# Performance work log

Hardware: AMD Instinct MI355X
Metric: run time of the kernel (lower is better)

The kernel has to match this reference:

```python
import jax, jax.numpy as jnp
import numpy as np

B, Tt, Ta, Tv = 2048, 128, 256, 256
D, E, R, H, L, NC = 64, 4, 8, 4, 4, 7
SCALING = 16.0 / 8.0  # alpha / r


def _ln(x, g, b, eps=1e-5):
    m = x.mean(-1, keepdims=True)
    v = ((x - m) ** 2).mean(-1, keepdims=True)
    return (x - m) / jnp.sqrt(v + eps) * g + b


def setup_inputs() -> dict:
    key = jax.random.key(0)
    ks = iter(jax.random.split(key, 64))
    def rn(shape, s=0.05):
        return jax.random.normal(next(ks), shape, jnp.float32) * s
    d = {}
    d['text'] = jax.random.normal(next(ks), (B, Tt, 300), jnp.float32)
    d['audio'] = jax.random.normal(next(ks), (B, Ta, 74), jnp.float32)
    d['video'] = jax.random.normal(next(ks), (B, Tv, 35), jnp.float32)
    # modality projections (Linear + LayerNorm)
    d['text_w'] = rn((300, D)); d['text_b'] = jnp.zeros(D); d['text_ln_g'] = jnp.ones(D); d['text_ln_b'] = jnp.zeros(D)
    d['audio_w'] = rn((74, D)); d['audio_b'] = jnp.zeros(D); d['audio_ln_g'] = jnp.ones(D); d['audio_ln_b'] = jnp.zeros(D)
    d['video_w'] = rn((35, D)); d['video_b'] = jnp.zeros(D); d['video_ln_g'] = jnp.ones(D); d['video_ln_b'] = jnp.zeros(D)
    d['latent'] = rn((1, L, D), 0.02)
    # cross-attention in/out projections
    d['wq'] = rn((D, D)); d['bq'] = jnp.zeros(D)
    d['wk'] = rn((D, D)); d['bk'] = jnp.zeros(D)
    d['wv'] = rn((D, D)); d['bv'] = jnp.zeros(D)
    d['wo'] = rn((D, D)); d['bo'] = jnp.zeros(D)
    d['n1_g'] = jnp.ones(D); d['n1_b'] = jnp.zeros(D)
    d['ffn_w1'] = rn((D, 4 * D)); d['ffn_b1'] = jnp.zeros(4 * D)
    d['ffn_w2'] = rn((4 * D, D)); d['ffn_b2'] = jnp.zeros(D)
    d['n2_g'] = jnp.ones(D); d['n2_b'] = jnp.zeros(D)
    # router
    d['r_w1'] = rn((D, D)); d['r_b1'] = jnp.zeros(D)
    d['r_ln_g'] = jnp.ones(D); d['r_ln_b'] = jnp.zeros(D)
    d['r_w2'] = rn((D, E)); d['r_b2'] = jnp.zeros(E)
    d['p1_w'] = rn((D, D // 2)); d['p1_b'] = jnp.zeros(D // 2)
    d['p2_w'] = rn((D, D // 2)); d['p2_b'] = jnp.zeros(D // 2)
    # LoRA experts, stacked: down [E,D,R], up [E,R,D]
    d['lora_down'] = rn((E, D, R), 0.1)
    d['lora_up'] = rn((E, R, D), 0.1)
    # classifier
    d['c_ln_g'] = jnp.ones(D); d['c_ln_b'] = jnp.zeros(D)
    d['c_w1'] = rn((D, D), 0.02); d['c_b1'] = jnp.zeros(D)
    d['c_w2'] = rn((D, NC), 0.02); d['c_b2'] = jnp.zeros(NC)
    return d


def reference(text, audio, video,
              text_w, text_b, text_ln_g, text_ln_b,
              audio_w, audio_b, audio_ln_g, audio_ln_b,
              video_w, video_b, video_ln_g, video_ln_b,
              latent, wq, bq, wk, bk, wv, bv, wo, bo,
              n1_g, n1_b, ffn_w1, ffn_b1, ffn_w2, ffn_b2, n2_g, n2_b,
              r_w1, r_b1, r_ln_g, r_ln_b, r_w2, r_b2,
              p1_w, p1_b, p2_w, p2_b,
              lora_down, lora_up,
              c_ln_g, c_ln_b, c_w1, c_b1, c_w2, c_b2):
    b = text.shape[0]
    def proj(x, w, bb, g, gb):  # Linear + LN + ReLU (dropout = eval identity)
        return jax.nn.relu(_ln(x @ w + bb, g, gb))
    # mean-pool each modality over time, project to d_model -> [b,3,D]
    zt = proj(text.mean(1), text_w, text_b, text_ln_g, text_ln_b)
    za = proj(audio.mean(1), audio_w, audio_b, audio_ln_g, audio_ln_b)
    zv = proj(video.mean(1), video_w, video_b, video_ln_g, video_ln_b)
    inputs = jnp.stack([zt, za, zv], axis=1)  # [b,3,D]
    lat = jnp.broadcast_to(latent, (b, L, D))
    # cross-attention: latent queries attend over 3 modality tokens
    hd = D // H
    q = (lat @ wq + bq).reshape(b, L, H, hd)
    k = (inputs @ wk + bk).reshape(b, -1, H, hd)
    v = (inputs @ wv + bv).reshape(b, -1, H, hd)
    scores = jnp.einsum('blhd,bshd->bhls', q, k) / jnp.sqrt(jnp.float32(hd))
    attn = jax.nn.softmax(scores, axis=-1)
    attn_out = jnp.einsum('bhls,bshd->blhd', attn, v).reshape(b, L, D) @ wo + bo
    lat = _ln(lat + attn_out, n1_g, n1_b)
    ffn = jax.nn.gelu(lat @ ffn_w1 + ffn_b1, approximate=False) @ ffn_w2 + ffn_b2
    lat = _ln(lat + ffn, n2_g, n2_b)
    f = lat.mean(1)  # [b,D] perceiver features
    # router
    r_logits = jax.nn.relu(_ln(f @ r_w1 + r_b1, r_ln_g, r_ln_b)) @ r_w2 + r_b2
    weights = jax.nn.softmax(r_logits, axis=-1)  # [b,E]
    view1 = f @ p1_w + p1_b
    view2 = f @ p2_w + p2_b
    # all LoRA experts as one batched grouped GEMM
    down = jnp.einsum('bd,edr->ber', f, lora_down)
    up = jnp.einsum('ber,erd->bed', down, lora_up) * SCALING
    expert_out = f[:, None, :] + up  # [b,E,D]
    fused = jnp.einsum('bed,be->bd', expert_out, weights)
    # classifier
    h = jax.nn.relu(_ln(fused, c_ln_g, c_ln_b) @ c_w1 + c_b1)
    logits = h @ c_w2 + c_b2
    return (logits, weights, fused, f, view1, view2)
```

## Files before the change

### kernel.cpp

```cpp
#include <hip/hip_runtime.h>
#include <math.h>
#include <string.h>

#define B_   2048
#define TT   128
#define TA   256
#define TV   256
#define CT   300
#define CA   74
#define CV   35
#define D    64
#define E_   4
#define R_   8
#define H_   4
#define L_   4
#define NC   7
#define POOLW 416

struct Params {
  const float *text, *audio, *video;
  const float *text_w, *text_b, *text_ln_g, *text_ln_b;
  const float *audio_w, *audio_b, *audio_ln_g, *audio_ln_b;
  const float *video_w, *video_b, *video_ln_g, *video_ln_b;
  const float *latent;
  const float *wq, *bq, *wk, *bk, *wv, *bv, *wo, *bo;
  const float *n1_g, *n1_b, *ffn_w1, *ffn_b1, *ffn_w2, *ffn_b2, *n2_g, *n2_b;
  const float *r_w1, *r_b1, *r_ln_g, *r_ln_b, *r_w2, *r_b2;
  const float *p1_w, *p1_b, *p2_w, *p2_b;
  const float *lora_down, *lora_up;
  const float *c_ln_g, *c_ln_b, *c_w1, *c_b1, *c_w2, *c_b2;
  float *out;
};

__device__ __forceinline__ float wsum(float v) {
#pragma unroll
  for (int m = 32; m >= 1; m >>= 1) v += __shfl_xor(v, m, 64);
  return v;
}
__device__ __forceinline__ float hsum16(float v) {
#pragma unroll
  for (int m = 8; m >= 1; m >>= 1) v += __shfl_xor(v, m, 64);
  return v;
}
#define WB() __builtin_amdgcn_wave_barrier()

__global__ __launch_bounds__(256) void fused_kernel(Params p) {
  const int tid = threadIdx.x;
  const int lane = tid & 63;
  const int w = tid >> 6;
  const int b0 = blockIdx.x * 4;
  const int b = b0 + w;

  __shared__ __align__(16) float4 sbufT[3][4][75];
  __shared__ __align__(8)  float2 sbufA[6][4][37];
  __shared__ float sbufV[7][4][35];
  __shared__ __align__(16) float s_pool[4][POOLW];
  __shared__ float s_q[L_ * D];
  __shared__ float s_z[4][3 * D];
  __shared__ float s_k[4][3 * D];
  __shared__ float s_ao[4][L_ * D];
  __shared__ float s_lat1[4][L_ * D];
  __shared__ float s_h1w[4][256];
  __shared__ float s_f[4][D];
  __shared__ float s_down[4][E_ * R_];
  __shared__ float s_cl[4][D];

  {
    const int c4 = tid % 75, g = tid / 75;
    if (g < 3) {
      float4 acc[4];
#pragma unroll
      for (int s = 0; s < 4; ++s) acc[s] = make_float4(0.f, 0.f, 0.f, 0.f);
      for (int t = g; t < TT; t += 3) {
#pragma unroll
        for (int s = 0; s < 4; ++s) {
          float4 v = *reinterpret_cast<const float4*>(
              p.text + (size_t)(b0 + s) * (TT * CT) + t * CT + 4 * c4);
          acc[s].x += v.x; acc[s].y += v.y; acc[s].z += v.z; acc[s].w += v.w;
        }
      }
#pragma unroll
      for (int s = 0; s < 4; ++s) sbufT[g][s][c4] = acc[s];
    }
  }
  {
    const int c2 = tid % 37, g = tid / 37;
    if (g < 6) {
      float2 acc[4];
#pragma unroll
      for (int s = 0; s < 4; ++s) acc[s] = make_float2(0.f, 0.f);
      for (int t = g; t < TA; t += 6) {
#pragma unroll
        for (int s = 0; s < 4; ++s) {
          float2 v = *reinterpret_cast<const float2*>(
              p.audio + (size_t)(b0 + s) * (TA * CA) + t * CA + 2 * c2);
          acc[s].x += v.x; acc[s].y += v.y;
        }
      }
#pragma unroll
      for (int s = 0; s < 4; ++s) sbufA[g][s][c2] = acc[s];
    }
  }
  {
    const int c = tid % 35, g = tid / 35;
    if (g < 7) {
      float acc[4] = {0.f, 0.f, 0.f, 0.f};
      for (int t = g; t < TV; t += 7) {
#pragma unroll
        for (int s = 0; s < 4; ++s)
          acc[s] += p.video[(size_t)(b0 + s) * (TV * CV) + t * CV + c];
      }
#pragma unroll
      for (int s = 0; s < 4; ++s) sbufV[g][s][c] = acc[s];
    }
  }
  {
    const int l = tid >> 6, j = tid & 63;
    float acc = p.bq[j];
    for (int i = 0; i < D; ++i) acc += p.latent[l * D + i] * p.wq[i * D + j];
    s_q[tid] = acc;
  }
  __syncthreads();

  if (tid < 75) {
#pragma unroll
    for (int s = 0; s < 4; ++s) {
      float4 a = sbufT[0][s][tid], bb = sbufT[1][s][tid], c = sbufT[2][s][tid];
      float4 r;
      r.x = (a.x + bb.x + c.x) * (1.f / TT);
      r.y = (a.y + bb.y + c.y) * (1.f / TT);
      r.z = (a.z + bb.z + c.z) * (1.f / TT);
      r.w = (a.w + bb.w + c.w) * (1.f / TT);
      *reinterpret_cast<float4*>(&s_pool[s][4 * tid]) = r;
    }
  } else if (tid < 112) {
    const int c2 = tid - 75;
#pragma unroll
    for (int s = 0; s < 4; ++s) {
      float2 r = make_float2(0.f, 0.f);
#pragma unroll
      for (int g = 0; g < 6; ++g) { float2 v = sbufA[g][s][c2]; r.x += v.x; r.y += v.y; }
      r.x *= (1.f / TA); r.y *= (1.f / TA);
      *reinterpret_cast<float2*>(&s_pool[s][CT + 2 * c2]) = r;
    }
  } else if (tid < 147) {
    const int c = tid - 112;
#pragma unroll
    for (int s = 0; s < 4; ++s) {
      float r = 0.f;
#pragma unroll
      for (int g = 0; g < 7; ++g) r += sbufV[g][s][c];
      s_pool[s][CT + CA + c] = r * (1.f / TV);
    }
  }
  __syncthreads();

  {
    float acc = p.text_b[lane];
    for (int i = 0; i < CT; ++i) acc += s_pool[w][i] * p.text_w[i * D + lane];
    float mu = wsum(acc) * (1.f / D);
    float d = acc - mu;
    float var = wsum(d * d) * (1.f / D);
    s_z[w][0 * D + lane] =
        fmaxf(d * rsqrtf(var + 1e-5f) * p.text_ln_g[lane] + p.text_ln_b[lane], 0.f);

    acc = p.audio_b[lane];
    for (int i = 0; i < CA; ++i) acc += s_pool[w][CT + i] * p.audio_w[i * D + lane];
    mu = wsum(acc) * (1.f / D); d = acc - mu; var = wsum(d * d) * (1.f / D);
    s_z[w][1 * D + lane] =
        fmaxf(d * rsqrtf(var + 1e-5f) * p.audio_ln_g[lane] + p.audio_ln_b[lane], 0.f);

    acc = p.video_b[lane];
    for (int i = 0; i < CV; ++i) acc += s_pool[w][CT + CA + i] * p.video_w[i * D + lane];
    mu = wsum(acc) * (1.f / D); d = acc - mu; var = wsum(d * d) * (1.f / D);
    s_z[w][2 * D + lane] =
        fmaxf(d * rsqrtf(var + 1e-5f) * p.video_ln_g[lane] + p.video_ln_b[lane], 0.f);
  }
  WB();

  float vreg[3];
#pragma unroll
  for (int s = 0; s < 3; ++s) {
    float ak = p.bk[lane], av = p.bv[lane];
    for (int i = 0; i < D; ++i) {
      float z = s_z[w][s * D + i];
      ak += z * p.wk[i * D + lane];
      av += z * p.wv[i * D + lane];
    }
    s_k[w][s * D + lane] = ak;
    vreg[s] = av;
  }
  WB();

  float aw[L_][3];
#pragma unroll
  for (int l = 0; l < L_; ++l) {
    float sc0 = hsum16(s_q[l * D + lane] * s_k[w][0 * D + lane]) * 0.25f;
    float sc1 = hsum16(s_q[l * D + lane] * s_k[w][1 * D + lane]) * 0.25f;
    float sc2 = hsum16(s_q[l * D + lane] * s_k[w][2 * D + lane]) * 0.25f;
    float mx = fmaxf(sc0, fmaxf(sc1, sc2));
    float e0 = expf(sc0 - mx), e1 = expf(sc1 - mx), e2 = expf(sc2 - mx);
    float inv = 1.f / (e0 + e1 + e2);
    aw[l][0] = e0 * inv; aw[l][1] = e1 * inv; aw[l][2] = e2 * inv;
  }

#pragma unroll
  for (int l = 0; l < L_; ++l)
    s_ao[w][l * D + lane] = aw[l][0] * vreg[0] + aw[l][1] * vreg[1] + aw[l][2] * vreg[2];
  WB();

#pragma unroll
  for (int l = 0; l < L_; ++l) {
    float acc = p.bo[lane];
    for (int i = 0; i < D; ++i) acc += s_ao[w][l * D + i] * p.wo[i * D + lane];
    float x = p.latent[l * D + lane] + acc;
    float mu = wsum(x) * (1.f / D);
    float d = x - mu;
    float var = wsum(d * d) * (1.f / D);
    s_lat1[w][l * D + lane] = d * rsqrtf(var + 1e-5f) * p.n1_g[lane] + p.n1_b[lane];
  }
  WB();

  float hacc[L_][4];
  {
#pragma unroll
    for (int k = 0; k < 4; ++k) {
      float bb = p.ffn_b1[k * 64 + lane];
#pragma unroll
      for (int l = 0; l < L_; ++l) hacc[l][k] = bb;
    }
    for (int i = 0; i < D; ++i) {
      float x0 = s_lat1[w][0 * D + i], x1 = s_lat1[w][1 * D + i];
      float x2 = s_lat1[w][2 * D + i], x3 = s_lat1[w][3 * D + i];
#pragma unroll
      for (int k = 0; k < 4; ++k) {
        float wv = p.ffn_w1[i * 256 + k * 64 + lane];
        hacc[0][k] += x0 * wv; hacc[1][k] += x1 * wv;
        hacc[2][k] += x2 * wv; hacc[3][k] += x3 * wv;
      }
    }
  }

  float fl;
  {
    float fsum = 0.f;
#pragma unroll
    for (int l = 0; l < L_; ++l) {
#pragma unroll
      for (int k = 0; k < 4; ++k) {
        float x = hacc[l][k];
        s_h1w[w][k * 64 + lane] = 0.5f * x * (1.f + erff(x * 0.70710678118654752f));
      }
      WB();
      float acc = p.ffn_b2[lane];
      for (int m2 = 0; m2 < 256; ++m2) acc += s_h1w[w][m2] * p.ffn_w2[m2 * D + lane];
      float x = s_lat1[w][l * D + lane] + acc;
      float mu = wsum(x) * (1.f / D);
      float d = x - mu;
      float var = wsum(d * d) * (1.f / D);
      fsum += d * rsqrtf(var + 1e-5f) * p.n2_g[lane] + p.n2_b[lane];
      WB();
    }
    fl = 0.25f * fsum;
    s_f[w][lane] = fl;
    p.out[(size_t)B_ * 75 + (size_t)b * D + lane] = fl;
  }
  WB();

  float w0, w1, w2, w3;
  {
    float acc = p.r_b1[lane];
    for (int i = 0; i < D; ++i) acc += s_f[w][i] * p.r_w1[i * D + lane];
    float mu = wsum(acc) * (1.f / D);
    float d = acc - mu;
    float var = wsum(d * d) * (1.f / D);
    float rr = fmaxf(d * rsqrtf(var + 1e-5f) * p.r_ln_g[lane] + p.r_ln_b[lane], 0.f);
    float l0 = wsum(rr * p.r_w2[lane * E_ + 0]) + p.r_b2[0];
    float l1 = wsum(rr * p.r_w2[lane * E_ + 1]) + p.r_b2[1];
    float l2 = wsum(rr * p.r_w2[lane * E_ + 2]) + p.r_b2[2];
    float l3 = wsum(rr * p.r_w2[lane * E_ + 3]) + p.r_b2[3];
    float mx = fmaxf(fmaxf(l0, l1), fmaxf(l2, l3));
    float e0 = expf(l0 - mx), e1 = expf(l1 - mx), e2 = expf(l2 - mx), e3 = expf(l3 - mx);
    float inv = 1.f / (e0 + e1 + e2 + e3);
    w0 = e0 * inv; w1 = e1 * inv; w2 = e2 * inv; w3 = e3 * inv;
    float wsel = (lane == 0) ? w0 : (lane == 1) ? w1 : (lane == 2) ? w2 : w3;
    if (lane < E_) p.out[(size_t)B_ * 7 + (size_t)b * E_ + lane] = wsel;
  }

  {
    const float* PW = (lane < 32) ? p.p1_w : p.p2_w;
    const float* PB = (lane < 32) ? p.p1_b : p.p2_b;
    const int col = lane & 31;
    float acc = PB[col];
    for (int i = 0; i < D; ++i) acc += s_f[w][i] * PW[i * 32 + col];
    const size_t base = (lane < 32) ? (size_t)B_ * 139 : (size_t)B_ * 171;
    p.out[base + (size_t)b * 32 + col] = acc;
  }

  if (lane < E_ * R_) {
    const int e = lane >> 3, r = lane & 7;
    float acc = 0.f;
    for (int dd = 0; dd < D; ++dd) acc += s_f[w][dd] * p.lora_down[e * D * R_ + dd * R_ + r];
    s_down[w][lane] = acc;
  }
  WB();

  float fused;
  {
    const float we4[4] = {w0, w1, w2, w3};
    float acc = 0.f;
#pragma unroll
    for (int e = 0; e < E_; ++e) {
      float up = 0.f;
#pragma unroll
      for (int r = 0; r < R_; ++r)
        up += s_down[w][e * R_ + r] * p.lora_up[e * R_ * D + r * D + lane];
      acc += we4[e] * (fl + 2.0f * up);
    }
    fused = acc;
    p.out[(size_t)B_ * 11 + (size_t)b * D + lane] = fused;
  }

  {
    float mu = wsum(fused) * (1.f / D);
    float d = fused - mu;
    float var = wsum(d * d) * (1.f / D);
    s_cl[w][lane] = d * rsqrtf(var + 1e-5f) * p.c_ln_g[lane] + p.c_ln_b[lane];
  }
  WB();
  {
    float acc = p.c_b1[lane];
    for (int i = 0; i < D; ++i) acc += s_cl[w][i] * p.c_w1[i * D + lane];
    float h = fmaxf(acc, 0.f);
#pragma unroll
    for (int nc = 0; nc < NC; ++nc) {
      float lg = wsum(h * p.c_w2[lane * NC + nc]) + p.c_b2[nc];
      if (lane == nc) p.out[(size_t)b * NC + nc] = lg;
    }
  }
}

extern "C" void kernel_launch(void* const* d_in, const int* in_sizes, int n_in,
                              void* d_out, int out_size, void* d_ws, size_t ws_size,
                              hipStream_t stream) {
  (void)in_sizes; (void)n_in; (void)out_size; (void)d_ws; (void)ws_size;
  Params p;
  memcpy(&p, d_in, 50 * sizeof(void*));
  p.out = (float*)d_out;
  fused_kernel<<<dim3(B_ / 4), dim3(256), 0, stream>>>(p);
}
```

Baseline: 698.9 us.

## Double block to 512 threads, split pooling and FFN work across eight waves

```diff
diff --git a/kernel.cpp b/kernel.cpp
--- a/kernel.cpp
+++ b/kernel.cpp
@@ -42,96 +42,184 @@
   for (int m = 8; m >= 1; m >>= 1) v += __shfl_xor(v, m, 64);
   return v;
 }
+__device__ __forceinline__ void acc4(float4& a, const float4 v) {
+  a.x += v.x; a.y += v.y; a.z += v.z; a.w += v.w;
+}
+__device__ __forceinline__ void acc2f(float2& a, const float2 v) { a.x += v.x; a.y += v.y; }
 #define WB() __builtin_amdgcn_wave_barrier()
 
-__global__ __launch_bounds__(256) void fused_kernel(Params p) {
+#define SBT(g, s, c)  sbufT[((g) * 4 + (s)) * 75 + (c)]
+#define SBA(g, s, c)  sbufA[((g) * 4 + (s)) * 37 + (c)]
+#define SBV(g, s, c)  sbufV[((g) * 4 + (s)) * 35 + (c)]
+#define SP(s, i)      s_pool[(s) * POOLW + (i)]
+#define SZI(s, i)     s_z[(s) * 192 + (i)]
+#define SKI(s, i)     s_k[(s) * 192 + (i)]
+#define SAO(s, i)     s_ao[(s) * 256 + (i)]
+#define SL1(s, i, l)  s_lat1T[(((s) * 64 + (i)) << 2) + (l)]
+#define SH1(s, c, l)  s_h1[(((s) * 256 + (c)) << 2) + (l)]
+#define SL2(s, l, j)  s_lat2[(((s) * 4 + (l)) << 6) + (j)]
+#define SF(s, i)      s_f[(s) * 64 + (i)]
+#define SDN(s, i)     s_down[(s) * 32 + (i)]
+#define SCL(s, i)     s_cl[(s) * 64 + (i)]
+
+__global__ __launch_bounds__(512, 4) void fused_kernel(Params p) {
   const int tid = threadIdx.x;
   const int lane = tid & 63;
   const int w = tid >> 6;
   const int b0 = blockIdx.x * 4;
-  const int b = b0 + w;
-
-  __shared__ __align__(16) float4 sbufT[3][4][75];
-  __shared__ __align__(8)  float2 sbufA[6][4][37];
-  __shared__ float sbufV[7][4][35];
-  __shared__ __align__(16) float s_pool[4][POOLW];
-  __shared__ float s_q[L_ * D];
-  __shared__ float s_z[4][3 * D];
-  __shared__ float s_k[4][3 * D];
-  __shared__ float s_ao[4][L_ * D];
-  __shared__ float s_lat1[4][L_ * D];
-  __shared__ float s_h1w[4][256];
-  __shared__ float s_f[4][D];
-  __shared__ float s_down[4][E_ * R_];
-  __shared__ float s_cl[4][D];
-
-  {
+
+  __shared__ __align__(16) unsigned char smem_raw[34304];
+  float4* const sbufT   = reinterpret_cast<float4*>(smem_raw);
+  float2* const sbufA   = reinterpret_cast<float2*>(smem_raw + 14400);
+  float*  const sbufV   = reinterpret_cast<float*>(smem_raw + 21504);
+  float*  const s_pool  = reinterpret_cast<float*>(smem_raw + 25424);
+  float*  const s_q     = reinterpret_cast<float*>(smem_raw + 33280);
+  float*  const s_z     = reinterpret_cast<float*>(smem_raw);
+  float*  const s_k     = reinterpret_cast<float*>(smem_raw + 3072);
+  float*  const s_ao    = reinterpret_cast<float*>(smem_raw + 6144);
+  float*  const s_lat1T = reinterpret_cast<float*>(smem_raw + 10240);
+  float*  const s_h1    = reinterpret_cast<float*>(smem_raw + 14336);
+  float*  const s_lat2  = reinterpret_cast<float*>(smem_raw + 6144);
+  float*  const s_f     = reinterpret_cast<float*>(smem_raw + 30720);
+  float*  const s_down  = reinterpret_cast<float*>(smem_raw + 31744);
+  float*  const s_cl    = reinterpret_cast<float*>(smem_raw + 32256);
+
+  if (tid < 256) {
     const int c4 = tid % 75, g = tid / 75;
     if (g < 3) {
-      float4 acc[4];
-#pragma unroll
-      for (int s = 0; s < 4; ++s) acc[s] = make_float4(0.f, 0.f, 0.f, 0.f);
-      for (int t = g; t < TT; t += 3) {
-#pragma unroll
-        for (int s = 0; s < 4; ++s) {
-          float4 v = *reinterpret_cast<const float4*>(
-              p.text + (size_t)(b0 + s) * (TT * CT) + t * CT + 4 * c4);
-          acc[s].x += v.x; acc[s].y += v.y; acc[s].z += v.z; acc[s].w += v.w;
-        }
-      }
-#pragma unroll
-      for (int s = 0; s < 4; ++s) sbufT[g][s][c4] = acc[s];
-    }
-  }
-  {
-    const int c2 = tid % 37, g = tid / 37;
-    if (g < 6) {
-      float2 acc[4];
-#pragma unroll
-      for (int s = 0; s < 4; ++s) acc[s] = make_float2(0.f, 0.f);
-      for (int t = g; t < TA; t += 6) {
-#pragma unroll
-        for (int s = 0; s < 4; ++s) {
-          float2 v = *reinterpret_cast<const float2*>(
-              p.audio + (size_t)(b0 + s) * (TA * CA) + t * CA + 2 * c2);
-          acc[s].x += v.x; acc[s].y += v.y;
-        }
-      }
-#pragma unroll
-      for (int s = 0; s < 4; ++s) sbufA[g][s][c2] = acc[s];
-    }
-  }
-  {
-    const int c = tid % 35, g = tid / 35;
-    if (g < 7) {
-      float acc[4] = {0.f, 0.f, 0.f, 0.f};
-      for (int t = g; t < TV; t += 7) {
-#pragma unroll
-        for (int s = 0; s < 4; ++s)
-          acc[s] += p.video[(size_t)(b0 + s) * (TV * CV) + t * CV + c];
-      }
-#pragma unroll
-      for (int s = 0; s < 4; ++s) sbufV[g][s][c] = acc[s];
-    }
-  }
-  {
-    const int l = tid >> 6, j = tid & 63;
-    float acc = p.bq[j];
-    for (int i = 0; i < D; ++i) acc += p.latent[l * D + i] * p.wq[i * D + j];
-    s_q[tid] = acc;
+      float4 accT[4];
+      const float* tp[4];
+#pragma unroll
+      for (int s = 0; s < 4; ++s) {
+        accT[s] = make_float4(0.f, 0.f, 0.f, 0.f);
+        tp[s] = p.text + (size_t)(b0 + s) * (TT * CT) + 4 * c4;
+      }
+      int t = g;
+      for (; t + 9 < TT; t += 12) {
+        float4 u[4][4];
+#pragma unroll
+        for (int s = 0; s < 4; ++s)
+#pragma unroll
+          for (int k = 0; k < 4; ++k)
+            u[s][k] = *reinterpret_cast<const float4*>(tp[s] + (size_t)(t + 3 * k) * CT);
+#pragma unroll
+        for (int s = 0; s < 4; ++s)
+#pragma unroll
+          for (int k = 0; k < 4; ++k) acc4(accT[s], u[s][k]);
+      }
+      for (; t + 3 < TT; t += 6) {
+        float4 u[4][2];
+#pragma unroll
+        for (int s = 0; s < 4; ++s)
+#pragma unroll
+          for (int k = 0; k < 2; ++k)
+            u[s][k] = *reinterpret_cast<const float4*>(tp[s] + (size_t)(t + 3 * k) * CT);
+#pragma unroll
+        for (int s = 0; s < 4; ++s) { acc4(accT[s], u[s][0]); acc4(accT[s], u[s][1]); }
+      }
+      for (; t < TT; t += 3) {
+#pragma unroll
+        for (int s = 0; s < 4; ++s)
+          acc4(accT[s], *reinterpret_cast<const float4*>(tp[s] + (size_t)t * CT));
+      }
+#pragma unroll
+      for (int s = 0; s < 4; ++s) SBT(g, s, c4) = accT[s];
+    }
+    {
+      const int l = tid >> 6, j = tid & 63;
+      float acc = p.bq[j];
+      for (int i = 0; i < D; ++i) acc += p.latent[l * D + i] * p.wq[i * D + j];
+      s_q[tid] = acc;
+    }
+  } else {
+    const int tid2 = tid - 256;
+    const int c2 = tid2 % 37, ga = tid2 / 37;
+    if (ga < 6) {
+      float2 accA[4];
+      const float* ap[4];
+#pragma unroll
+      for (int s = 0; s < 4; ++s) {
+        accA[s] = make_float2(0.f, 0.f);
+        ap[s] = p.audio + (size_t)(b0 + s) * (TA * CA) + 2 * c2;
+      }
+      int t = ga;
+      for (; t + 18 < TA; t += 24) {
+        float2 u[4][4];
+#pragma unroll
+        for (int s = 0; s < 4; ++s)
+#pragma unroll
+          for (int k = 0; k < 4; ++k)
+            u[s][k] = *reinterpret_cast<const float2*>(ap[s] + (size_t)(t + 6 * k) * CA);
+#pragma unroll
+        for (int s = 0; s < 4; ++s)
+#pragma unroll
+          for (int k = 0; k < 4; ++k) acc2f(accA[s], u[s][k]);
+      }
+      for (; t + 6 < TA; t += 12) {
+        float2 u[4][2];
+#pragma unroll
+        for (int s = 0; s < 4; ++s)
+#pragma unroll
+          for (int k = 0; k < 2; ++k)
+            u[s][k] = *reinterpret_cast<const float2*>(ap[s] + (size_t)(t + 6 * k) * CA);
+#pragma unroll
+        for (int s = 0; s < 4; ++s) { acc2f(accA[s], u[s][0]); acc2f(accA[s], u[s][1]); }
+      }
+      for (; t < TA; t += 6) {
+#pragma unroll
+        for (int s = 0; s < 4; ++s)
+          acc2f(accA[s], *reinterpret_cast<const float2*>(ap[s] + (size_t)t * CA));
+      }
+#pragma unroll
+      for (int s = 0; s < 4; ++s) SBA(ga, s, c2) = accA[s];
+    }
+    const int cv = tid2 % 35, gv = tid2 / 35;
+    if (gv < 7) {
+      float accV[4] = {0.f, 0.f, 0.f, 0.f};
+      const float* vp[4];
+#pragma unroll
+      for (int s = 0; s < 4; ++s) vp[s] = p.video + (size_t)(b0 + s) * (TV * CV) + cv;
+      int t = gv;
+      for (; t + 21 < TV; t += 28) {
+        float u[4][4];
+#pragma unroll
+        for (int s = 0; s < 4; ++s)
+#pragma unroll
+          for (int k = 0; k < 4; ++k) u[s][k] = vp[s][(size_t)(t + 7 * k) * CV];
+#pragma unroll
+        for (int s = 0; s < 4; ++s)
+#pragma unroll
+          for (int k = 0; k < 4; ++k) accV[s] += u[s][k];
+      }
+      for (; t + 7 < TV; t += 14) {
+        float u[4][2];
+#pragma unroll
+        for (int s = 0; s < 4; ++s)
+#pragma unroll
+          for (int k = 0; k < 2; ++k) u[s][k] = vp[s][(size_t)(t + 7 * k) * CV];
+#pragma unroll
+        for (int s = 0; s < 4; ++s) { accV[s] += u[s][0]; accV[s] += u[s][1]; }
+      }
+      for (; t < TV; t += 7) {
+#pragma unroll
+        for (int s = 0; s < 4; ++s) accV[s] += vp[s][(size_t)t * CV];
+      }
+#pragma unroll
+      for (int s = 0; s < 4; ++s) SBV(gv, s, cv) = accV[s];
+    }
   }
   __syncthreads();
 
   if (tid < 75) {
 #pragma unroll
     for (int s = 0; s < 4; ++s) {
-      float4 a = sbufT[0][s][tid], bb = sbufT[1][s][tid], c = sbufT[2][s][tid];
+      float4 a = SBT(0, s, tid), bb = SBT(1, s, tid), c = SBT(2, s, tid);
       float4 r;
       r.x = (a.x + bb.x + c.x) * (1.f / TT);
       r.y = (a.y + bb.y + c.y) * (1.f / TT);
       r.z = (a.z + bb.z + c.z) * (1.f / TT);
       r.w = (a.w + bb.w + c.w) * (1.f / TT);
-      *reinterpret_cast<float4*>(&s_pool[s][4 * tid]) = r;
+      *reinterpret_cast<float4*>(&SP(s, 4 * tid)) = r;
     }
   } else if (tid < 112) {
     const int c2 = tid - 75;
@@ -139,9 +227,9 @@
     for (int s = 0; s < 4; ++s) {
       float2 r = make_float2(0.f, 0.f);
 #pragma unroll
-      for (int g = 0; g < 6; ++g) { float2 v = sbufA[g][s][c2]; r.x += v.x; r.y += v.y; }
+      for (int g = 0; g < 6; ++g) acc2f(r, SBA(g, s, c2));
       r.x *= (1.f / TA); r.y *= (1.f / TA);
-      *reinterpret_cast<float2*>(&s_pool[s][CT + 2 * c2]) = r;
+      *reinterpret_cast<float2*>(&SP(s, CT + 2 * c2)) = r;
     }
   } else if (tid < 147) {
     const int c = tid - 112;
@@ -149,193 +237,229 @@
     for (int s = 0; s < 4; ++s) {
       float r = 0.f;
 #pragma unroll
-      for (int g = 0; g < 7; ++g) r += sbufV[g][s][c];
-      s_pool[s][CT + CA + c] = r * (1.f / TV);
-    }
-  }
-  __syncthreads();
-
-  {
-    float acc = p.text_b[lane];
-    for (int i = 0; i < CT; ++i) acc += s_pool[w][i] * p.text_w[i * D + lane];
-    float mu = wsum(acc) * (1.f / D);
-    float d = acc - mu;
-    float var = wsum(d * d) * (1.f / D);
-    s_z[w][0 * D + lane] =
-        fmaxf(d * rsqrtf(var + 1e-5f) * p.text_ln_g[lane] + p.text_ln_b[lane], 0.f);
-
-    acc = p.audio_b[lane];
-    for (int i = 0; i < CA; ++i) acc += s_pool[w][CT + i] * p.audio_w[i * D + lane];
-    mu = wsum(acc) * (1.f / D); d = acc - mu; var = wsum(d * d) * (1.f / D);
-    s_z[w][1 * D + lane] =
-        fmaxf(d * rsqrtf(var + 1e-5f) * p.audio_ln_g[lane] + p.audio_ln_b[lane], 0.f);
-
-    acc = p.video_b[lane];
-    for (int i = 0; i < CV; ++i) acc += s_pool[w][CT + CA + i] * p.video_w[i * D + lane];
-    mu = wsum(acc) * (1.f / D); d = acc - mu; var = wsum(d * d) * (1.f / D);
-    s_z[w][2 * D + lane] =
-        fmaxf(d * rsqrtf(var + 1e-5f) * p.video_ln_g[lane] + p.video_ln_b[lane], 0.f);
-  }
-  WB();
-
-  float vreg[3];
-#pragma unroll
-  for (int s = 0; s < 3; ++s) {
-    float ak = p.bk[lane], av = p.bv[lane];
-    for (int i = 0; i < D; ++i) {
-      float z = s_z[w][s * D + i];
-      ak += z * p.wk[i * D + lane];
-      av += z * p.wv[i * D + lane];
-    }
-    s_k[w][s * D + lane] = ak;
-    vreg[s] = av;
-  }
-  WB();
-
-  float aw[L_][3];
-#pragma unroll
-  for (int l = 0; l < L_; ++l) {
-    float sc0 = hsum16(s_q[l * D + lane] * s_k[w][0 * D + lane]) * 0.25f;
-    float sc1 = hsum16(s_q[l * D + lane] * s_k[w][1 * D + lane]) * 0.25f;
-    float sc2 = hsum16(s_q[l * D + lane] * s_k[w][2 * D + lane]) * 0.25f;
-    float mx = fmaxf(sc0, fmaxf(sc1, sc2));
-    float e0 = expf(sc0 - mx), e1 = expf(sc1 - mx), e2 = expf(sc2 - mx);
-    float inv = 1.f / (e0 + e1 + e2);
-    aw[l][0] = e0 * inv; aw[l][1] = e1 * inv; aw[l][2] = e2 * inv;
-  }
-
-#pragma unroll
-  for (int l = 0; l < L_; ++l)
-    s_ao[w][l * D + lane] = aw[l][0] * vreg[0] + aw[l][1] * vreg[1] + aw[l][2] * vreg[2];
-  WB();
-
-#pragma unroll
-  for (int l = 0; l < L_; ++l) {
-    float acc = p.bo[lane];
-    for (int i = 0; i < D; ++i) acc += s_ao[w][l * D + i] * p.wo[i * D + lane];
-    float x = p.latent[l * D + lane] + acc;
-    float mu = wsum(x) * (1.f / D);
-    float d = x - mu;
-    float var = wsum(d * d) * (1.f / D);
-    s_lat1[w][l * D + lane] = d * rsqrtf(var + 1e-5f) * p.n1_g[lane] + p.n1_b[lane];
-  }
-  WB();
-
-  float hacc[L_][4];
-  {
-#pragma unroll
-    for (int k = 0; k < 4; ++k) {
-      float bb = p.ffn_b1[k * 64 + lane];
-#pragma unroll
-      for (int l = 0; l < L_; ++l) hacc[l][k] = bb;
-    }
-    for (int i = 0; i < D; ++i) {
-      float x0 = s_lat1[w][0 * D + i], x1 = s_lat1[w][1 * D + i];
-      float x2 = s_lat1[w][2 * D + i], x3 = s_lat1[w][3 * D + i];
-#pragma unroll
-      for (int k = 0; k < 4; ++k) {
-        float wv = p.ffn_w1[i * 256 + k * 64 + lane];
-        hacc[0][k] += x0 * wv; hacc[1][k] += x1 * wv;
-        hacc[2][k] += x2 * wv; hacc[3][k] += x3 * wv;
-      }
-    }
-  }
-
-  float fl;
-  {
-    float fsum = 0.f;
+      for (int g = 0; g < 7; ++g) r += SBV(g, s, c);
+      SP(s, CT + CA + c) = r * (1.f / TV);
+    }
+  }
+  __syncthreads();
+
+  float fl = 0.f, w0 = 0.f, w1 = 0.f, w2 = 0.f, w3 = 0.f;
+
+  if (w < 4) {
+    const int b = b0 + w;
+    (void)b;
+    {
+      float acc = p.text_b[lane];
+#pragma unroll 4
+      for (int i = 0; i < CT; ++i) acc += SP(w, i) * p.text_w[i * D + lane];
+      float mu = wsum(acc) * (1.f / D);
+      float d = acc - mu;
+      float var = wsum(d * d) * (1.f / D);
+      SZI(w, 0 * D + lane) =
+          fmaxf(d * rsqrtf(var + 1e-5f) * p.text_ln_g[lane] + p.text_ln_b[lane], 0.f);
+
+      acc = p.audio_b[lane];
+#pragma unroll 4
+      for (int i = 0; i < CA; ++i) acc += SP(w, CT + i) * p.audio_w[i * D + lane];
+      mu = wsum(acc) * (1.f / D); d = acc - mu; var = wsum(d * d) * (1.f / D);
+      SZI(w, 1 * D + lane) =
+          fmaxf(d * rsqrtf(var + 1e-5f) * p.audio_ln_g[lane] + p.audio_ln_b[lane], 0.f);
+
+      acc = p.video_b[lane];
+#pragma unroll 4
+      for (int i = 0; i < CV; ++i) acc += SP(w, CT + CA + i) * p.video_w[i * D + lane];
+      mu = wsum(acc) * (1.f / D); d = acc - mu; var = wsum(d * d) * (1.f / D);
+      SZI(w, 2 * D + lane) =
+          fmaxf(d * rsqrtf(var + 1e-5f) * p.video_ln_g[lane] + p.video_ln_b[lane], 0.f);
+    }
+    WB();
+
+    float vreg[3];
+#pragma unroll
+    for (int s = 0; s < 3; ++s) {
+      float ak = p.bk[lane], av = p.bv[lane];
+#pragma unroll 4
+      for (int i = 0; i < D; ++i) {
+        float z = SZI(w, s * D + i);
+        ak += z * p.wk[i * D + lane];
+        av += z * p.wv[i * D + lane];
+      }
+      SKI(w, s * D + lane) = ak;
+      vreg[s] = av;
+    }
+    WB();
+
+    float aw[L_][3];
 #pragma unroll
     for (int l = 0; l < L_; ++l) {
-#pragma unroll
-      for (int k = 0; k < 4; ++k) {
-        float x = hacc[l][k];
-        s_h1w[w][k * 64 + lane] = 0.5f * x * (1.f + erff(x * 0.70710678118654752f));
-      }
-      WB();
-      float acc = p.ffn_b2[lane];
-      for (int m2 = 0; m2 < 256; ++m2) acc += s_h1w[w][m2] * p.ffn_w2[m2 * D + lane];
-      float x = s_lat1[w][l * D + lane] + acc;
+      float sc0 = hsum16(s_q[l * D + lane] * SKI(w, 0 * D + lane)) * 0.25f;
+      float sc1 = hsum16(s_q[l * D + lane] * SKI(w, 1 * D + lane)) * 0.25f;
+      float sc2 = hsum16(s_q[l * D + lane] * SKI(w, 2 * D + lane)) * 0.25f;
+      float mx = fmaxf(sc0, fmaxf(sc1, sc2));
+      float e0 = expf(sc0 - mx), e1 = expf(sc1 - mx), e2 = expf(sc2 - mx);
+      float inv = 1.f / (e0 + e1 + e2);
+      aw[l][0] = e0 * inv; aw[l][1] = e1 * inv; aw[l][2] = e2 * inv;
+    }
+
+#pragma unroll
+    for (int l = 0; l < L_; ++l)
+      SAO(w, l * D + lane) = aw[l][0] * vreg[0] + aw[l][1] * vreg[1] + aw[l][2] * vreg[2];
+    WB();
+
+    float zl1[4];
+#pragma unroll
+    for (int l = 0; l < L_; ++l) {
+      float acc = p.bo[lane];
+#pragma unroll 4
+      for (int i = 0; i < D; ++i) acc += SAO(w, l * D + i) * p.wo[i * D + lane];
+      float x = p.latent[l * D + lane] + acc;
       float mu = wsum(x) * (1.f / D);
       float d = x - mu;
       float var = wsum(d * d) * (1.f / D);
-      fsum += d * rsqrtf(var + 1e-5f) * p.n2_g[lane] + p.n2_b[lane];
-      WB();
-    }
-    fl = 0.25f * fsum;
-    s_f[w][lane] = fl;
+      zl1[l] = d * rsqrtf(var + 1e-5f) * p.n1_g[lane] + p.n1_b[lane];
+    }
+    *reinterpret_cast<float4*>(&SL1(w, lane, 0)) = make_float4(zl1[0], zl1[1], zl1[2], zl1[3]);
+  }
+  __syncthreads();
+
+  {
+    const int g2 = tid >> 8, c = tid & 255;
+    float facc[2][4];
+    const float bb1 = p.ffn_b1[c];
+#pragma unroll
+    for (int sp = 0; sp < 2; ++sp)
+#pragma unroll
+      for (int l = 0; l < 4; ++l) facc[sp][l] = bb1;
+#pragma unroll 2
+    for (int i = 0; i < D; ++i) {
+      float w1v = p.ffn_w1[i * 256 + c];
+#pragma unroll
+      for (int sp = 0; sp < 2; ++sp) {
+        float4 xl = *reinterpret_cast<const float4*>(&SL1(2 * g2 + sp, i, 0));
+        facc[sp][0] += xl.x * w1v;
+        facc[sp][1] += xl.y * w1v;
+        facc[sp][2] += xl.z * w1v;
+        facc[sp][3] += xl.w * w1v;
+      }
+    }
+#pragma unroll
+    for (int sp = 0; sp < 2; ++sp) {
+      float4 hv;
+      hv.x = 0.5f * facc[sp][0] * (1.f + erff(facc[sp][0] * 0.70710678118654752f));
+      hv.y = 0.5f * facc[sp][1] * (1.f + erff(facc[sp][1] * 0.70710678118654752f));
+      hv.z = 0.5f * facc[sp][2] * (1.f + erff(facc[sp][2] * 0.70710678118654752f));
+      hv.w = 0.5f * facc[sp][3] * (1.f + erff(facc[sp][3] * 0.70710678118654752f));
+      *reinterpret_cast<float4*>(&SH1(2 * g2 + sp, c, 0)) = hv;
+    }
+  }
+  __syncthreads();
+
+  {
+    const int l = w & 3, g2 = w >> 2;
+    float acc2[2];
+    acc2[0] = p.ffn_b2[lane];
+    acc2[1] = p.ffn_b2[lane];
+#pragma unroll 4
+    for (int m2 = 0; m2 < 256; ++m2) {
+      float w2v = p.ffn_w2[m2 * D + lane];
+      acc2[0] += SH1(2 * g2 + 0, m2, l) * w2v;
+      acc2[1] += SH1(2 * g2 + 1, m2, l) * w2v;
+    }
+#pragma unroll
+    for (int sp = 0; sp < 2; ++sp) {
+      const int s = 2 * g2 + sp;
+      float x = SL1(s, lane, l) + acc2[sp];
+      float mu = wsum(x) * (1.f / D);
+      float d = x - mu;
+      float var = wsum(d * d) * (1.f / D);
+      SL2(s, l, lane) = d * rsqrtf(var + 1e-5f) * p.n2_g[lane] + p.n2_b[lane];
+    }
+  }
+  __syncthreads();
+
+  if (w < 4) {
+    const int b = b0 + w;
+    fl = 0.25f * (((SL2(w, 0, lane) + SL2(w, 1, lane)) + SL2(w, 2, lane)) + SL2(w, 3, lane));
+    SF(w, lane) = fl;
     p.out[(size_t)B_ * 75 + (size_t)b * D + lane] = fl;
   }
-  WB();
-
-  float w0, w1, w2, w3;
-  {
-    float acc = p.r_b1[lane];
-    for (int i = 0; i < D; ++i) acc += s_f[w][i] * p.r_w1[i * D + lane];
-    float mu = wsum(acc) * (1.f / D);
-    float d = acc - mu;
-    float var = wsum(d * d) * (1.f / D);
-    float rr = fmaxf(d * rsqrtf(var + 1e-5f) * p.r_ln_g[lane] + p.r_ln_b[lane], 0.f);
-    float l0 = wsum(rr * p.r_w2[lane * E_ + 0]) + p.r_b2[0];
-    float l1 = wsum(rr * p.r_w2[lane * E_ + 1]) + p.r_b2[1];
-    float l2 = wsum(rr * p.r_w2[lane * E_ + 2]) + p.r_b2[2];
-    float l3 = wsum(rr * p.r_w2[lane * E_ + 3]) + p.r_b2[3];
-    float mx = fmaxf(fmaxf(l0, l1), fmaxf(l2, l3));
-    float e0 = expf(l0 - mx), e1 = expf(l1 - mx), e2 = expf(l2 - mx), e3 = expf(l3 - mx);
-    float inv = 1.f / (e0 + e1 + e2 + e3);
-    w0 = e0 * inv; w1 = e1 * inv; w2 = e2 * inv; w3 = e3 * inv;
-    float wsel = (lane == 0) ? w0 : (lane == 1) ? w1 : (lane == 2) ? w2 : w3;
-    if (lane < E_) p.out[(size_t)B_ * 7 + (size_t)b * E_ + lane] = wsel;
-  }
-
-  {
+  __syncthreads();
+
+  if (w >= 4) {
+    const int sv = w - 4;
+    const int bs = b0 + sv;
     const float* PW = (lane < 32) ? p.p1_w : p.p2_w;
     const float* PB = (lane < 32) ? p.p1_b : p.p2_b;
     const int col = lane & 31;
     float acc = PB[col];
-    for (int i = 0; i < D; ++i) acc += s_f[w][i] * PW[i * 32 + col];
+#pragma unroll 4
+    for (int i = 0; i < D; ++i) acc += SF(sv, i) * PW[i * 32 + col];
     const size_t base = (lane < 32) ? (size_t)B_ * 139 : (size_t)B_ * 171;
-    p.out[base + (size_t)b * 32 + col] = acc;
-  }
-
-  if (lane < E_ * R_) {
-    const int e = lane >> 3, r = lane & 7;
-    float acc = 0.f;
-    for (int dd = 0; dd < D; ++dd) acc += s_f[w][dd] * p.lora_down[e * D * R_ + dd * R_ + r];
-    s_down[w][lane] = acc;
-  }
-  WB();
-
-  float fused;
-  {
-    const float we4[4] = {w0, w1, w2, w3};
-    float acc = 0.f;
-#pragma unroll
-    for (int e = 0; e < E_; ++e) {
-      float up = 0.f;
-#pragma unroll
-      for (int r = 0; r < R_; ++r)
-        up += s_down[w][e * R_ + r] * p.lora_up[e * R_ * D + r * D + lane];
-      acc += we4[e] * (fl + 2.0f * up);
-    }
-    fused = acc;
-    p.out[(size_t)B_ * 11 + (size_t)b * D + lane] = fused;
-  }
-
-  {
-    float mu = wsum(fused) * (1.f / D);
-    float d = fused - mu;
-    float var = wsum(d * d) * (1.f / D);
-    s_cl[w][lane] = d * rsqrtf(var + 1e-5f) * p.c_ln_g[lane] + p.c_ln_b[lane];
-  }
-  WB();
-  {
-    float acc = p.c_b1[lane];
-    for (int i = 0; i < D; ++i) acc += s_cl[w][i] * p.c_w1[i * D + lane];
-    float h = fmaxf(acc, 0.f);
-#pragma unroll
-    for (int nc = 0; nc < NC; ++nc) {
-      float lg = wsum(h * p.c_w2[lane * NC + nc]) + p.c_b2[nc];
-      if (lane == nc) p.out[(size_t)b * NC + nc] = lg;
+    p.out[base + (size_t)bs * 32 + col] = acc;
+  } else {
+    const int b = b0 + w;
+    {
+      float acc = p.r_b1[lane];
+#pragma unroll 4
+      for (int i = 0; i < D; ++i) acc += SF(w, i) * p.r_w1[i * D + lane];
+      float mu = wsum(acc) * (1.f / D);
+      float d = acc - mu;
+      float var = wsum(d * d) * (1.f / D);
+      float rr = fmaxf(d * rsqrtf(var + 1e-5f) * p.r_ln_g[lane] + p.r_ln_b[lane], 0.f);
+      float l0 = wsum(rr * p.r_w2[lane * E_ + 0]) + p.r_b2[0];
+      float l1 = wsum(rr * p.r_w2[lane * E_ + 1]) + p.r_b2[1];
+      float l2 = wsum(rr * p.r_w2[lane * E_ + 2]) + p.r_b2[2];
+      float l3 = wsum(rr * p.r_w2[lane * E_ + 3]) + p.r_b2[3];
+      float mx = fmaxf(fmaxf(l0, l1), fmaxf(l2, l3));
+      float e0 = expf(l0 - mx), e1 = expf(l1 - mx), e2 = expf(l2 - mx), e3 = expf(l3 - mx);
+      float inv = 1.f / (e0 + e1 + e2 + e3);
+      w0 = e0 * inv; w1 = e1 * inv; w2 = e2 * inv; w3 = e3 * inv;
+      float wsel = (lane == 0) ? w0 : (lane == 1) ? w1 : (lane == 2) ? w2 : w3;
+      if (lane < E_) p.out[(size_t)B_ * 7 + (size_t)b * E_ + lane] = wsel;
+    }
+
+    if (lane < E_ * R_) {
+      const int e = lane >> 3, r = lane & 7;
+      float acc = 0.f;
+#pragma unroll 4
+      for (int dd = 0; dd < D; ++dd) acc += SF(w, dd) * p.lora_down[e * D * R_ + dd * R_ + r];
+      SDN(w, lane) = acc;
+    }
+    WB();
+
+    float fused;
+    {
+      const float we4[4] = {w0, w1, w2, w3};
+      float acc = 0.f;
+#pragma unroll
+      for (int e = 0; e < E_; ++e) {
+        float up = 0.f;
+#pragma unroll
+        for (int r = 0; r < R_; ++r)
+          up += SDN(w, e * R_ + r) * p.lora_up[e * R_ * D + r * D + lane];
+        acc += we4[e] * (fl + 2.0f * up);
+      }
+      fused = acc;
+      p.out[(size_t)B_ * 11 + (size_t)b * D + lane] = fused;
+    }
+
+    {
+      float mu = wsum(fused) * (1.f / D);
+      float d = fused - mu;
+      float var = wsum(d * d) * (1.f / D);
+      SCL(w, lane) = d * rsqrtf(var + 1e-5f) * p.c_ln_g[lane] + p.c_ln_b[lane];
+    }
+    WB();
+    {
+      float acc = p.c_b1[lane];
+#pragma unroll 4
+      for (int i = 0; i < D; ++i) acc += SCL(w, i) * p.c_w1[i * D + lane];
+      float h = fmaxf(acc, 0.f);
+#pragma unroll
+      for (int nc = 0; nc < NC; ++nc) {
+        float lg = wsum(h * p.c_w2[lane * NC + nc]) + p.c_b2[nc];
+        if (lane == nc) p.out[(size_t)b * NC + nc] = lg;
+      }
     }
   }
 }
@@ -347,5 +471,5 @@
   Params p;
   memcpy(&p, d_in, 50 * sizeof(void*));
   p.out = (float*)d_out;
-  fused_kernel<<<dim3(B_ / 4), dim3(256), 0, stream>>>(p);
+  fused_kernel<<<dim3(B_ / 4), dim3(512), 0, stream>>>(p);
 }
```

Measured after the change: 749.1 us. +7.2%, slower.
